# Optimization experiments

Measured on AMD Instinct MI355X. Metric: run time of the kernel, lower is better.

Reference implementation:

```python
import jax, jax.numpy as jnp
import numpy as np

# Config (decoder-only Transformer)
NL, H, D, DK, V, B, S = 6, 16, 1024, 64, 32000, 2, 1024  # DK = d_v = D // H
DFF = 4 * D


def _layer_norm(x, g, b, eps=1e-5):
    mu = jnp.mean(x, axis=-1, keepdims=True)
    var = jnp.mean(jnp.square(x - mu), axis=-1, keepdims=True)
    return (x - mu) * jax.lax.rsqrt(var + eps) * g + b


def _pos_encoding(seq_len, d_embed):
    # Matches PositionalEncoding: base 1000 (as in source), sin at even i, cos at odd i
    pos = jnp.arange(seq_len, dtype=jnp.float32)[:, None]
    i = jnp.arange(d_embed, dtype=jnp.float32)[None, :]
    angle = pos / jnp.power(1000.0, i / d_embed)
    return jnp.where((jnp.arange(d_embed)[None, :] % 2) == 0, jnp.sin(angle), jnp.cos(angle))


def setup_inputs() -> dict:
    key = jax.random.key(0)
    ks = jax.random.split(key, 8)
    n = lambda k, shp, sc: jax.random.normal(k, shp, dtype=jnp.float32) * sc
    return {
        "outputs": jax.random.randint(ks[0], (B, S), 0, V),
        "embed": n(ks[1], (V, D), 0.02),
        # per-head Q/K/V projections stacked over layers and heads: [NL, H, D, DK]
        "Wq": n(ks[2], (NL, H, D, DK), D ** -0.5),
        "Wk": n(ks[3], (NL, H, D, DK), D ** -0.5),
        "Wv": n(ks[4], (NL, H, D, DK), D ** -0.5),
        "W1": n(ks[5], (NL, D, DFF), D ** -0.5),
        "W2": n(ks[6], (NL, DFF, D), DFF ** -0.5),
        "ln1_g": jnp.ones((NL, D), jnp.float32),
        "ln1_b": jnp.zeros((NL, D), jnp.float32),
        "ln2_g": jnp.ones((NL, D), jnp.float32),
        "ln2_b": jnp.zeros((NL, D), jnp.float32),
        "Wout": n(ks[7], (D, V), D ** -0.5),
        "bout": jnp.zeros((V,), jnp.float32),
    }


def reference(outputs, embed, Wq, Wk, Wv, W1, W2, ln1_g, ln1_b, ln2_g, ln2_b, Wout, bout):
    x = embed[outputs]                      # [B, S, D]
    x = x + _pos_encoding(S, D)
    scale = jnp.float32(DK ** 0.5)
    for l in range(NL):
        # Masked multi-head self-attention (per-head projections batched over H)
        q = jnp.einsum('bsd,hdk->bhsk', x, Wq[l])
        k = jnp.einsum('bsd,hdk->bhsk', x, Wk[l])
        v = jnp.einsum('bsd,hdk->bhsk', x, Wv[l])
        scores = jnp.einsum('bhqk,bhsk->bhqs', q, k) / scale   # [B,H,S,S]
        # Faithful to source: tril then masked_fill(score == 0, -inf)
        scores = jnp.tril(scores)
        scores = jnp.where(scores == 0, -jnp.inf, scores)
        w = jax.nn.softmax(scores, axis=-1)
        attn = jnp.einsum('bhqs,bhsv->bqhv', w, v).reshape(B, S, H * DK)
        x = _layer_norm(x + attn, ln1_g[l], ln1_b[l])
        # Position-wise FFN (dropout is identity at inference)
        h = jax.nn.relu(x @ W1[l]) @ W2[l]
        x = _layer_norm(x + h, ln2_g[l], ln2_b[l])
    return x @ Wout + bout                  # logits [B, S, V]
```

## Files before the change

### kernel.cpp

```cpp
#include <hip/hip_runtime.h>

typedef unsigned short u16;
typedef __attribute__((ext_vector_type(8))) short short8;
typedef __attribute__((ext_vector_type(4))) float f32x4;

#define NLAYER 6
#define NH 16
#define DMODEL 1024
#define DHEAD 64
#define NVOCAB 32000
#define NB 2
#define NS 1024
#define NDFF 4096
#define MTOK (NB*NS)

__device__ __forceinline__ u16 f2b(float f) {
    union { float f; unsigned u; } x; x.f = f;
    unsigned r = x.u + 0x7fffu + ((x.u >> 16) & 1u);
    return (u16)(r >> 16);
}

#define GLL16(gp, lp) __builtin_amdgcn_global_load_lds( \
    (const __attribute__((address_space(1))) void*)(gp), \
    (__attribute__((address_space(3))) void*)(lp), 16, 0, 0)

__global__ void transpose_cvt(const float* __restrict__ src, u16* __restrict__ dst,
                              int R, int C, long srcStride, long dstStride)
{
    __shared__ float t[32][33];
    const int c0 = blockIdx.x * 32, r0 = blockIdx.y * 32;
    const float* s = src + (long)blockIdx.z * srcStride;
    u16* d = dst + (long)blockIdx.z * dstStride;
    const int tx = threadIdx.x, ty = threadIdx.y;
    #pragma unroll
    for (int j = 0; j < 32; j += 8)
        t[ty + j][tx] = s[(long)(r0 + ty + j) * C + c0 + tx];
    __syncthreads();
    #pragma unroll
    for (int j = 0; j < 32; j += 8)
        d[(long)(c0 + ty + j) * R + r0 + tx] = f2b(t[tx][ty + j]);
}

__global__ void transpose_qkv(const float* __restrict__ src, u16* __restrict__ dst, int sel)
{
    __shared__ float t[32][33];
    const int bi = blockIdx.z, l = bi >> 4, h = bi & 15;
    const float* s = src + (long)bi * (DMODEL * DHEAD);
    u16* d = dst + (long)l * 3072 * DMODEL + (long)(sel * 1024 + h * 64) * DMODEL;
    const int c0 = blockIdx.x * 32, r0 = blockIdx.y * 32;
    const int tx = threadIdx.x, ty = threadIdx.y;
    #pragma unroll
    for (int j = 0; j < 32; j += 8)
        t[ty + j][tx] = s[(long)(r0 + ty + j) * DHEAD + c0 + tx];
    __syncthreads();
    #pragma unroll
    for (int j = 0; j < 32; j += 8)
        d[(long)(c0 + ty + j) * DMODEL + r0 + tx] = f2b(t[tx][ty + j]);
}

__global__ void embed_pe(const int* __restrict__ toks, const float* __restrict__ emb,
                         float* __restrict__ x, u16* __restrict__ xb)
{
    const int row = blockIdx.x;
    const int s = row & (NS - 1);
    const long erow = (long)toks[row] * DMODEL;
    const long base = (long)row * DMODEL;
    #pragma unroll
    for (int j = 0; j < 4; ++j) {
        int d = threadIdx.x + j * 256;
        float ang = (float)s * exp2f(-(float)d * (9.965784284662087f / 1024.f));
        float pe = (d & 1) ? cosf(ang) : sinf(ang);
        float v = emb[erow + d] + pe;
        x[base + d] = v;
        xb[base + d] = f2b(v);
    }
}

template<int ND>
__global__ __launch_bounds__(256) void ln_residual(
    const float* __restrict__ xin, const float* __restrict__ delta,
    const float* __restrict__ delta2,
    const float* __restrict__ g, const float* __restrict__ bb,
    float* __restrict__ xout, u16* __restrict__ xbout)
{
    __shared__ float red[8];
    const long base = (long)blockIdx.x * DMODEL;
    float v[4]; float sum = 0.f, sq = 0.f;
    #pragma unroll
    for (int j = 0; j < 4; ++j) {
        int d = threadIdx.x + j * 256;
        float t = xin[base + d] + delta[base + d];
        if (ND == 2) t += delta2[base + d];
        v[j] = t; sum += t; sq += t * t;
    }
    #pragma unroll
    for (int off = 1; off < 64; off <<= 1) {
        sum += __shfl_xor(sum, off, 64);
        sq  += __shfl_xor(sq,  off, 64);
    }
    const int wv = threadIdx.x >> 6, lane = threadIdx.x & 63;
    if (lane == 0) { red[wv] = sum; red[4 + wv] = sq; }
    __syncthreads();
    float ts = red[0] + red[1] + red[2] + red[3];
    float tq = red[4] + red[5] + red[6] + red[7];
    float mu = ts * (1.f / DMODEL);
    float var = tq * (1.f / DMODEL) - mu * mu;
    float rstd = rsqrtf(var + 1e-5f);
    #pragma unroll
    for (int j = 0; j < 4; ++j) {
        int d = threadIdx.x + j * 256;
        float y = (v[j] - mu) * rstd * g[d] + bb[d];
        xout[base + d] = y;
        xbout[base + d] = f2b(y);
    }
}

template<int BM, int EPI>
__global__ __launch_bounds__(BM*2, 2) void gemm_pipe(
    const u16* __restrict__ A, const u16* __restrict__ Bt,
    void* __restrict__ Cout, const float* __restrict__ bias,
    int M, int N, int K, int lda, int ldb, size_t zstride)
{
    constexpr int WAVES = BM / 32;
    constexpr int WC = WAVES / 2;
    constexpr int MR = BM / 32;
    constexpr int TILE = BM * 32;

    __shared__ __align__(16) u16 As[4][TILE];
    __shared__ __align__(16) u16 Bs[4][TILE];

    const int nmb = M / BM;
    {
    }
    const int id = blockIdx.x, nwg = gridDim.x;
    const int q = nwg >> 3, r = nwg & 7, xcd = id & 7, loc = id >> 3;
    const int swz = (xcd < r ? xcd * (q + 1) : r * (q + 1) + (xcd - r) * q) + loc;
    const int m0 = (swz % nmb) * BM, n0 = (swz / nmb) * BM;
    const int koff = blockIdx.y * K;

    const int tid = threadIdx.x, wv = tid >> 6, lane = tid & 63;
    const int wr = wv / WC, wc = wv % WC;
    const int lrow = lane & 15, ks = lane >> 4;

    const u16* gsrc[4];
    int ldso[2];
    {
        const int l4 = lane >> 2, s = lane & 3;
        #pragma unroll
        for (int j = 0; j < 2; ++j) {
            const int row = j * (WAVES * 16) + wv * 16 + l4;
            const int x = (row >> 1) & 3;
            gsrc[j]     = A  + (size_t)(m0 + row) * lda + koff + (size_t)((s ^ x) * 8);
            gsrc[2 + j] = Bt + (size_t)(n0 + row) * ldb + koff + (size_t)((s ^ x) * 8);
            ldso[j] = (j * (WAVES * 16) + wv * 16) * 32;
        }
    }
    int aoff[MR], boff[4];
    #pragma unroll
    for (int m = 0; m < MR; ++m) {
        const int row = wr * (BM / 2) + m * 16 + lrow;
        aoff[m] = row * 32 + ((ks ^ ((row >> 1) & 3)) * 8);
    }
    #pragma unroll
    for (int n = 0; n < 4; ++n) {
        const int row = wc * 64 + n * 16 + lrow;
        boff[n] = row * 32 + ((ks ^ ((row >> 1) & 3)) * 8);
    }

    const int NT = K / 32;
    auto ISSUE = [&](int t) {
        const int b = t & 3;
        const size_t ko = (size_t)t * 32;
        #pragma unroll
        for (int j = 0; j < 2; ++j) {
            GLL16(gsrc[j] + ko,     &As[b][ldso[j]]);
            GLL16(gsrc[2 + j] + ko, &Bs[b][ldso[j]]);
        }
    };

    f32x4 acc[MR][4] = {};
    ISSUE(0); ISSUE(1); ISSUE(2);

    for (int t = 0; t < NT; ++t) {
        if (t < NT - 2)       { asm volatile("s_waitcnt vmcnt(8)" ::: "memory"); }
        else if (t == NT - 2) { asm volatile("s_waitcnt vmcnt(4)" ::: "memory"); }
        else                  { asm volatile("s_waitcnt vmcnt(0)" ::: "memory"); }
        __builtin_amdgcn_sched_barrier(0);
        __builtin_amdgcn_s_barrier();
        __builtin_amdgcn_sched_barrier(0);

        const int b = t & 3;
        short8 af[MR], bf[4];
        #pragma unroll
        for (int m = 0; m < MR; ++m) af[m] = *(const short8*)(&As[b][aoff[m]]);
        #pragma unroll
        for (int n = 0; n < 4; ++n)  bf[n] = *(const short8*)(&Bs[b][boff[n]]);
        if (t + 3 < NT) ISSUE(t + 3);
        __builtin_amdgcn_s_setprio(1);
        #pragma unroll
        for (int m = 0; m < MR; ++m)
            #pragma unroll
            for (int n = 0; n < 4; ++n)
                acc[m][n] = __builtin_amdgcn_mfma_f32_16x16x32_bf16(af[m], bf[n], acc[m][n], 0, 0, 0);
        __builtin_amdgcn_s_setprio(0);
    }

    #pragma unroll
    for (int m = 0; m < MR; ++m) {
        const int rr = m0 + wr * (BM / 2) + m * 16 + ks * 4;
        #pragma unroll
        for (int n = 0; n < 4; ++n) {
            const int cc = n0 + wc * 64 + n * 16 + lrow;
            if (EPI == 0) {
                float* C = (float*)Cout + (size_t)blockIdx.y * zstride;
                #pragma unroll
                for (int i = 0; i < 4; ++i) C[(size_t)(rr + i) * N + cc] = acc[m][n][i];
            } else if (EPI == 3) {
                float* C = (float*)Cout;
                const float bv = bias[cc];
                #pragma unroll
                for (int i = 0; i < 4; ++i) C[(size_t)(rr + i) * N + cc] = acc[m][n][i] + bv;
            } else {
                u16* C = (u16*)Cout;
                #pragma unroll
                for (int i = 0; i < 4; ++i) {
                    float vv = acc[m][n][i];
                    if (EPI == 2) vv = fmaxf(vv, 0.f);
                    C[(size_t)(rr + i) * N + cc] = f2b(vv);
                }
            }
        }
    }
}

__global__ __launch_bounds__(256, 2) void attn_flash(
    const u16* __restrict__ qkv, float* __restrict__ delta)
{
    __shared__ __align__(16) u16 Qs[64 * 64];
    __shared__ __align__(16) u16 Ks[64 * 64];
    __shared__ __align__(16) u16 Vts[64 * 64];
    __shared__ __align__(16) u16 Ps[4][16 * 64];

    const int pair = blockIdx.x, h = blockIdx.y, b = blockIdx.z;
    const int tid = threadIdx.x, wv = tid >> 6, lane = tid & 63;
    const int lrow = lane & 15, lk8 = (lane >> 4) * 8, li4 = (lane >> 4) * 4;
    const long base = (long)b * NS * 3072;

    for (int rep = 0; rep < 2; ++rep) {
        const int qt = rep == 0 ? pair : 15 - pair;
        __syncthreads();

        #pragma unroll
        for (int i = 0; i < 2; ++i) {
            int c0 = (wv * 2 + i) * 64;
            int c = c0 + lane;
            int row = c >> 3, col = (c & 7) * 8;
            GLL16(qkv + base + (long)(qt * 64 + row) * 3072 + h * 64 + col, Qs + c0 * 8);
        }

        f32x4 o[4] = {};
        float m_[4], l_[4];
        #pragma unroll
        for (int i = 0; i < 4; ++i) { m_[i] = -__builtin_inff(); l_[i] = 0.f; }

        for (int t = 0; t <= qt; ++t) {
            __syncthreads();
            #pragma unroll
            for (int i = 0; i < 2; ++i) {
                int c0 = (wv * 2 + i) * 64;
                int c = c0 + lane;
                int row = c >> 3, col = (c & 7) * 8;
                GLL16(qkv + base + (long)(t * 64 + row) * 3072 + 1024 + h * 64 + col, Ks + c0 * 8);
            }
            #pragma unroll
            for (int i = 0; i < 2; ++i) {
                int c = tid + i * 256;
                int kv = c >> 3, d0 = (c & 7) * 8;
                short8 vv = *(const short8*)(qkv + base + (long)(t * 64 + kv) * 3072 + 2048 + h * 64 + d0);
                #pragma unroll
                for (int j = 0; j < 8; ++j) Vts[(d0 + j) * 64 + kv] = ((u16*)&vv)[j];
            }
            __syncthreads();

            short8 aq[2];
            aq[0] = *(const short8*)(Qs + (wv * 16 + lrow) * 64 + lk8);
            aq[1] = *(const short8*)(Qs + (wv * 16 + lrow) * 64 + 32 + lk8);
            f32x4 sa[4];
            #pragma unroll
            for (int nb = 0; nb < 4; ++nb) {
                f32x4 z = {};
                #pragma unroll
                for (int kd = 0; kd < 2; ++kd) {
                    short8 bk = *(const short8*)(Ks + (nb * 16 + lrow) * 64 + kd * 32 + lk8);
                    z = __builtin_amdgcn_mfma_f32_16x16x32_bf16(aq[kd], bk, z, 0, 0, 0);
                }
                sa[nb] = z;
            }
            const int qrow0 = qt * 64 + wv * 16 + li4;
            #pragma unroll
            for (int nb = 0; nb < 4; ++nb)
                #pragma unroll
                for (int i = 0; i < 4; ++i) {
                    float sc = sa[nb][i] * 0.125f;
                    if (t == qt) {
                        int kvc = t * 64 + nb * 16 + lrow;
                        if (kvc > qrow0 + i) sc = -__builtin_inff();
                    }
                    sa[nb][i] = sc;
                }
            float mt[4];
            #pragma unroll
            for (int i = 0; i < 4; ++i)
                mt[i] = fmaxf(fmaxf(sa[0][i], sa[1][i]), fmaxf(sa[2][i], sa[3][i]));
            #pragma unroll
            for (int off = 1; off < 16; off <<= 1)
                #pragma unroll
                for (int i = 0; i < 4; ++i) mt[i] = fmaxf(mt[i], __shfl_xor(mt[i], off, 64));
            float fac[4], rs[4];
            #pragma unroll
            for (int i = 0; i < 4; ++i) {
                float mn = fmaxf(m_[i], mt[i]);
                fac[i] = expf(m_[i] - mn);
                m_[i] = mn;
                rs[i] = 0.f;
            }
            #pragma unroll
            for (int nb = 0; nb < 4; ++nb)
                #pragma unroll
                for (int i = 0; i < 4; ++i) {
                    float p = expf(sa[nb][i] - m_[i]);
                    sa[nb][i] = p; rs[i] += p;
                }
            #pragma unroll
            for (int off = 1; off < 16; off <<= 1)
                #pragma unroll
                for (int i = 0; i < 4; ++i) rs[i] += __shfl_xor(rs[i], off, 64);
            #pragma unroll
            for (int i = 0; i < 4; ++i) l_[i] = l_[i] * fac[i] + rs[i];
            #pragma unroll
            for (int nd = 0; nd < 4; ++nd)
                #pragma unroll
                for (int i = 0; i < 4; ++i) o[nd][i] *= fac[i];

            u16* ps = &Ps[wv][0];
            #pragma unroll
            for (int nb = 0; nb < 4; ++nb)
                #pragma unroll
                for (int i = 0; i < 4; ++i)
                    ps[(li4 + i) * 64 + nb * 16 + lrow] = f2b(sa[nb][i]);
            short8 pa[2];
            pa[0] = *(const short8*)(ps + lrow * 64 + lk8);
            pa[1] = *(const short8*)(ps + lrow * 64 + 32 + lk8);
            #pragma unroll
            for (int nd = 0; nd < 4; ++nd)
                #pragma unroll
                for (int kd = 0; kd < 2; ++kd) {
                    short8 vb = *(const short8*)(Vts + (nd * 16 + lrow) * 64 + kd * 32 + lk8);
                    o[nd] = __builtin_amdgcn_mfma_f32_16x16x32_bf16(pa[kd], vb, o[nd], 0, 0, 0);
                }
        }

        #pragma unroll
        for (int i = 0; i < 4; ++i) {
            const long row = (long)b * NS + qt * 64 + wv * 16 + li4 + i;
            const float inv = 1.f / l_[i];
            #pragma unroll
            for (int nd = 0; nd < 4; ++nd)
                delta[row * DMODEL + h * 64 + nd * 16 + lrow] = o[nd][i] * inv;
        }
    }
}

extern "C" void kernel_launch(void* const* d_in, const int* in_sizes, int n_in,
                              void* d_out, int out_size, void* d_ws, size_t ws_size,
                              hipStream_t stream) {
    const int*   toks  = (const int*)d_in[0];
    const float* emb   = (const float*)d_in[1];
    const float* Wq    = (const float*)d_in[2];
    const float* Wk    = (const float*)d_in[3];
    const float* Wv    = (const float*)d_in[4];
    const float* W1    = (const float*)d_in[5];
    const float* W2    = (const float*)d_in[6];
    const float* ln1g  = (const float*)d_in[7];
    const float* ln1b  = (const float*)d_in[8];
    const float* ln2g  = (const float*)d_in[9];
    const float* ln2b  = (const float*)d_in[10];
    const float* Wout  = (const float*)d_in[11];
    const float* bout  = (const float*)d_in[12];

    char* p = (char*)d_ws;
    auto alloc = [&](size_t bytes) { void* r = (void*)p; p += (bytes + 255) & ~(size_t)255; return r; };
    u16*   Wqkv_t = (u16*)alloc((size_t)NLAYER * 3072 * 1024 * 2);
    u16*   W1t    = (u16*)alloc((size_t)NLAYER * 4096 * 1024 * 2);
    u16*   W2t    = (u16*)alloc((size_t)NLAYER * 1024 * 4096 * 2);
    u16*   Woutt  = (u16*)alloc((size_t)NVOCAB * 1024 * 2);
    float* x      = (float*)alloc((size_t)MTOK * 1024 * 4);
    u16*   xb     = (u16*)alloc((size_t)MTOK * 1024 * 2);
    u16*   qkv    = (u16*)alloc((size_t)MTOK * 3072 * 2);
    u16*   hbuf   = (u16*)alloc((size_t)MTOK * 4096 * 2);
    float* dbuf   = (float*)alloc((size_t)MTOK * 1024 * 4);

    float* hbufF = (float*)hbuf;
    float* part2 = (float*)qkv;
    const size_t zstride = (size_t)(part2 - dbuf);

    dim3 tb(32, 8);
    transpose_qkv<<<dim3(2, 32, 96), tb, 0, stream>>>(Wq, Wqkv_t, 0);
    transpose_qkv<<<dim3(2, 32, 96), tb, 0, stream>>>(Wk, Wqkv_t, 1);
    transpose_qkv<<<dim3(2, 32, 96), tb, 0, stream>>>(Wv, Wqkv_t, 2);
    transpose_cvt<<<dim3(128, 32, 6), tb, 0, stream>>>(W1, W1t, 1024, 4096, 1024l * 4096, 4096l * 1024);
    transpose_cvt<<<dim3(32, 128, 6), tb, 0, stream>>>(W2, W2t, 4096, 1024, 4096l * 1024, 1024l * 4096);
    transpose_cvt<<<dim3(1000, 32, 1), tb, 0, stream>>>(Wout, Woutt, 1024, NVOCAB, 0, 0);

    embed_pe<<<MTOK, 256, 0, stream>>>(toks, emb, x, xb);

    for (int l = 0; l < NLAYER; ++l) {
        gemm_pipe<128, 1><<<dim3(16 * 24), 256, 0, stream>>>(
            xb, Wqkv_t + (size_t)l * 3072 * 1024, qkv, nullptr, MTOK, 3072, 1024, 1024, 1024, 0);
        attn_flash<<<dim3(8, NH, NB), 256, 0, stream>>>(qkv, hbufF);
        ln_residual<1><<<MTOK, 256, 0, stream>>>(x, hbufF, nullptr,
            ln1g + l * 1024, ln1b + l * 1024, x, xb);
        gemm_pipe<128, 2><<<dim3(16 * 32), 256, 0, stream>>>(
            xb, W1t + (size_t)l * 4096 * 1024, hbuf, nullptr, MTOK, 4096, 1024, 1024, 1024, 0);
        gemm_pipe<128, 0><<<dim3(16 * 8, 2), 256, 0, stream>>>(
            hbuf, W2t + (size_t)l * 1024 * 4096, dbuf, nullptr, MTOK, 1024, 2048, 4096, 4096, zstride);
        ln_residual<2><<<MTOK, 256, 0, stream>>>(x, dbuf, part2,
            ln2g + l * 1024, ln2b + l * 1024, x, xb);
    }

    gemm_pipe<256, 3><<<dim3(8 * 125), 512, 0, stream>>>(
        xb, Woutt, (float*)d_out, bout, MTOK, NVOCAB, 1024, 1024, 1024, 0);
}
```

Measured before the change: 1.305 ms.

## Double-buffer attention K/V with swizzled LDS, add dedicated vocab GEMM, vectorize transposes

Attention now double-buffers K and V tiles in LDS. The next tile's loads are prefetched into registers and the global-to-LDS path while the current tile computes, and XOR swizzling is applied to Q/K/V/P to avoid bank conflicts. A new 256x256 GEMM kernel for the output projection splits each k-step into two half-phases, interleaving B-tile prefetch with MFMAs and raising wave priority around the MFMA blocks. Weight transposes use 64x64 tiles with float4 loads and 16-byte stores. The added waitcnt and barrier choreography is intricate and could hide ordering bugs or raise register pressure.

New measurement: 1.451 ms. +11.1%, slower.

```diff
diff --git a/kernel.cpp b/kernel.cpp
--- a/kernel.cpp
+++ b/kernel.cpp
@@ -24,21 +24,34 @@
     (const __attribute__((address_space(1))) void*)(gp), \
     (__attribute__((address_space(3))) void*)(lp), 16, 0, 0)
 
-__global__ void transpose_cvt(const float* __restrict__ src, u16* __restrict__ dst,
-                              int R, int C, long srcStride, long dstStride)
+__global__ __launch_bounds__(256) void trans64(
+    const float* __restrict__ src, u16* __restrict__ dst,
+    int R, int C, long sStride, long dStride)
 {
-    __shared__ float t[32][33];
-    const int c0 = blockIdx.x * 32, r0 = blockIdx.y * 32;
-    const float* s = src + (long)blockIdx.z * srcStride;
-    u16* d = dst + (long)blockIdx.z * dstStride;
-    const int tx = threadIdx.x, ty = threadIdx.y;
-    #pragma unroll
-    for (int j = 0; j < 32; j += 8)
-        t[ty + j][tx] = s[(long)(r0 + ty + j) * C + c0 + tx];
+    __shared__ float sh[64][65];
+    const int c0 = blockIdx.x * 64, r0 = blockIdx.y * 64;
+    const float* s = src + (long)blockIdx.z * sStride;
+    u16* d = dst + (long)blockIdx.z * dStride;
+    const int tid = threadIdx.x;
+    const int lr = tid >> 4, lc = (tid & 15) * 4;
+    #pragma unroll
+    for (int q = 0; q < 4; ++q) {
+        const float4 v = *(const float4*)(s + (long)(r0 + q * 16 + lr) * C + c0 + lc);
+        sh[q * 16 + lr][lc + 0] = v.x;
+        sh[q * 16 + lr][lc + 1] = v.y;
+        sh[q * 16 + lr][lc + 2] = v.z;
+        sh[q * 16 + lr][lc + 3] = v.w;
+    }
     __syncthreads();
     #pragma unroll
-    for (int j = 0; j < 32; j += 8)
-        d[(long)(c0 + ty + j) * R + r0 + tx] = f2b(t[tx][ty + j]);
+    for (int k = 0; k < 2; ++k) {
+        const int t = tid + 256 * k;
+        const int col = t >> 3, rch = (t & 7) * 8;
+        u16 tmp[8];
+        #pragma unroll
+        for (int j = 0; j < 8; ++j) tmp[j] = f2b(sh[rch + j][col]);
+        *(short8*)(d + (long)(c0 + col) * R + r0 + rch) = *(const short8*)tmp;
+    }
 }
 
 __global__ void transpose_qkv(const float* __restrict__ src, u16* __restrict__ dst, int sel)
@@ -130,8 +143,6 @@
     __shared__ __align__(16) u16 Bs[4][TILE];
 
     const int nmb = M / BM;
-    {
-    }
     const int id = blockIdx.x, nwg = gridDim.x;
     const int q = nwg >> 3, r = nwg & 7, xcd = id & 7, loc = id >> 3;
     const int swz = (xcd < r ? xcd * (q + 1) : r * (q + 1) + (xcd - r) * q) + loc;
@@ -233,17 +244,126 @@
     }
 }
 
-__global__ __launch_bounds__(256, 2) void attn_flash(
+__global__ __launch_bounds__(512, 2) void gemm256(
+    const u16* __restrict__ A, const u16* __restrict__ Bt,
+    float* __restrict__ C, const float* __restrict__ bias,
+    int M, int N, int K)
+{
+    __shared__ __align__(16) u16 As[4][256 * 32];
+    __shared__ __align__(16) u16 Bs[4][256 * 32];
+
+    const int nmb = M >> 8;
+    const int id = blockIdx.x, nwg = gridDim.x;
+    const int q = nwg >> 3, r = nwg & 7, xcd = id & 7, loc = id >> 3;
+    const int swz = (xcd < r ? xcd * (q + 1) : r * (q + 1) + (xcd - r) * q) + loc;
+    const int m0 = (swz % nmb) * 256, n0 = (swz / nmb) * 256;
+
+    const int tid = threadIdx.x, wv = tid >> 6, lane = tid & 63;
+    const int wr = wv >> 2, wc = wv & 3;
+    const int lrow = lane & 15, ks = lane >> 4;
+
+    const u16* srcA[2]; const u16* srcB[2]; int dsto[2];
+    #pragma unroll
+    for (int i = 0; i < 2; ++i) {
+        const int c = (wv * 2 + i) * 64 + lane;
+        const int row = c >> 2, up = c & 3;
+        const int u = up ^ ((row >> 1) & 3);
+        srcA[i] = A  + (size_t)(m0 + row) * K + u * 8;
+        srcB[i] = Bt + (size_t)(n0 + row) * K + u * 8;
+        dsto[i] = c * 8;
+    }
+    int aoff[8], boff[4];
+    #pragma unroll
+    for (int m = 0; m < 8; ++m) {
+        const int row = wr * 128 + m * 16 + lrow;
+        aoff[m] = row * 32 + ((ks ^ ((row >> 1) & 3)) * 8);
+    }
+    #pragma unroll
+    for (int n = 0; n < 4; ++n) {
+        const int row = wc * 64 + n * 16 + lrow;
+        boff[n] = row * 32 + ((ks ^ ((row >> 1) & 3)) * 8);
+    }
+
+    const int NT = K >> 5;
+    for (int t = 0; t < 3; ++t) {
+        const int b = t & 3;
+        #pragma unroll
+        for (int i = 0; i < 2; ++i) GLL16(srcA[i] + t * 32, &As[b][dsto[i]]);
+        #pragma unroll
+        for (int i = 0; i < 2; ++i) GLL16(srcB[i] + t * 32, &Bs[b][dsto[i]]);
+    }
+
+    f32x4 acc[8][4] = {};
+    for (int t = 0; t < NT; ++t) {
+        const int b = t & 3, bs = (t + 3) & 3;
+        if (t < NT - 2)       { asm volatile("s_waitcnt vmcnt(8)" ::: "memory"); }
+        else if (t == NT - 2) { asm volatile("s_waitcnt vmcnt(4)" ::: "memory"); }
+        else                  { asm volatile("s_waitcnt vmcnt(0)" ::: "memory"); }
+        __builtin_amdgcn_sched_barrier(0);
+        __builtin_amdgcn_s_barrier();
+        __builtin_amdgcn_sched_barrier(0);
+
+        short8 af[4], bf[4];
+        #pragma unroll
+        for (int m = 0; m < 4; ++m) af[m] = *(const short8*)(&As[b][aoff[m]]);
+        #pragma unroll
+        for (int n = 0; n < 4; ++n) bf[n] = *(const short8*)(&Bs[b][boff[n]]);
+        if (t + 3 < NT) {
+            #pragma unroll
+            for (int i = 0; i < 2; ++i) GLL16(srcA[i] + (t + 3) * 32, &As[bs][dsto[i]]);
+        }
+        __builtin_amdgcn_s_setprio(1);
+        #pragma unroll
+        for (int m = 0; m < 4; ++m)
+            #pragma unroll
+            for (int n = 0; n < 4; ++n)
+                acc[m][n] = __builtin_amdgcn_mfma_f32_16x16x32_bf16(af[m], bf[n], acc[m][n], 0, 0, 0);
+        __builtin_amdgcn_s_setprio(0);
+
+        __builtin_amdgcn_sched_barrier(0);
+        __builtin_amdgcn_s_barrier();
+        __builtin_amdgcn_sched_barrier(0);
+
+        short8 af2[4];
+        #pragma unroll
+        for (int m = 0; m < 4; ++m) af2[m] = *(const short8*)(&As[b][aoff[4 + m]]);
+        if (t + 3 < NT) {
+            #pragma unroll
+            for (int i = 0; i < 2; ++i) GLL16(srcB[i] + (t + 3) * 32, &Bs[bs][dsto[i]]);
+        }
+        __builtin_amdgcn_s_setprio(1);
+        #pragma unroll
+        for (int m = 0; m < 4; ++m)
+            #pragma unroll
+            for (int n = 0; n < 4; ++n)
+                acc[4 + m][n] = __builtin_amdgcn_mfma_f32_16x16x32_bf16(af2[m], bf[n], acc[4 + m][n], 0, 0, 0);
+        __builtin_amdgcn_s_setprio(0);
+    }
+
+    #pragma unroll
+    for (int m = 0; m < 8; ++m) {
+        const int rr = m0 + wr * 128 + m * 16 + ks * 4;
+        #pragma unroll
+        for (int n = 0; n < 4; ++n) {
+            const int cc = n0 + wc * 64 + n * 16 + lrow;
+            const float bv = bias[cc];
+            #pragma unroll
+            for (int i = 0; i < 4; ++i) C[(size_t)(rr + i) * N + cc] = acc[m][n][i] + bv;
+        }
+    }
+}
+
+__global__ __launch_bounds__(256, 3) void attn_flash2(
     const u16* __restrict__ qkv, float* __restrict__ delta)
 {
     __shared__ __align__(16) u16 Qs[64 * 64];
-    __shared__ __align__(16) u16 Ks[64 * 64];
-    __shared__ __align__(16) u16 Vts[64 * 64];
+    __shared__ __align__(16) u16 Kd[2][64 * 64];
+    __shared__ __align__(16) u16 Vd[2][64 * 64];
     __shared__ __align__(16) u16 Ps[4][16 * 64];
 
     const int pair = blockIdx.x, h = blockIdx.y, b = blockIdx.z;
     const int tid = threadIdx.x, wv = tid >> 6, lane = tid & 63;
-    const int lrow = lane & 15, lk8 = (lane >> 4) * 8, li4 = (lane >> 4) * 4;
+    const int lrow = lane & 15, ks4 = lane >> 4, li4 = ks4 * 4;
     const long base = (long)b * NS * 3072;
 
     for (int rep = 0; rep < 2; ++rep) {
@@ -252,10 +372,44 @@
 
         #pragma unroll
         for (int i = 0; i < 2; ++i) {
-            int c0 = (wv * 2 + i) * 64;
-            int c = c0 + lane;
-            int row = c >> 3, col = (c & 7) * 8;
-            GLL16(qkv + base + (long)(qt * 64 + row) * 3072 + h * 64 + col, Qs + c0 * 8);
+            const int c = (wv * 2 + i) * 64 + lane;
+            const int row = c >> 3, u = (c & 7) ^ (row & 7);
+            GLL16(qkv + base + (long)(qt * 64 + row) * 3072 + h * 64 + u * 8, Qs + c * 8);
+        }
+        short8 vreg[2];
+        #pragma unroll
+        for (int i = 0; i < 2; ++i) {
+            const int c = tid + 256 * i;
+            vreg[i] = *(const short8*)(qkv + base + (long)(c >> 3) * 3072 + 2048 + h * 64 + (c & 7) * 8);
+        }
+        #pragma unroll
+        for (int i = 0; i < 2; ++i) {
+            const int c = (wv * 2 + i) * 64 + lane;
+            const int row = c >> 3, u = (c & 7) ^ (row & 7);
+            GLL16(qkv + base + (long)(row) * 3072 + 1024 + h * 64 + u * 8, Kd[0] + c * 8);
+        }
+        asm volatile("s_waitcnt vmcnt(4)" ::: "memory");
+        __builtin_amdgcn_sched_barrier(0);
+        __builtin_amdgcn_s_barrier();
+        __builtin_amdgcn_sched_barrier(0);
+        short8 aq[2];
+        {
+            const int row = wv * 16 + lrow;
+            aq[0] = *(const short8*)(Qs + row * 64 + ((ks4 ^ (row & 7)) * 8));
+            aq[1] = *(const short8*)(Qs + row * 64 + (((4 + ks4) ^ (row & 7)) * 8));
+        }
+        asm volatile("s_waitcnt vmcnt(2)" ::: "memory");
+        __builtin_amdgcn_sched_barrier(0);
+        #pragma unroll
+        for (int i = 0; i < 2; ++i) {
+            const int c = tid + 256 * i;
+            const int kv = c >> 3, d0 = (c & 7) * 8;
+            #pragma unroll
+            for (int jj = 0; jj < 8; ++jj) {
+                const int j = jj ^ (lane & 7);
+                const int row = d0 + j;
+                Vd[0][row * 64 + (((kv >> 3) ^ (row & 7)) * 8) + (kv & 7)] = ((const u16*)&vreg[i])[j];
+            }
         }
 
         f32x4 o[4] = {};
@@ -264,34 +418,39 @@
         for (int i = 0; i < 4; ++i) { m_[i] = -__builtin_inff(); l_[i] = 0.f; }
 
         for (int t = 0; t <= qt; ++t) {
-            __syncthreads();
-            #pragma unroll
-            for (int i = 0; i < 2; ++i) {
-                int c0 = (wv * 2 + i) * 64;
-                int c = c0 + lane;
-                int row = c >> 3, col = (c & 7) * 8;
-                GLL16(qkv + base + (long)(t * 64 + row) * 3072 + 1024 + h * 64 + col, Ks + c0 * 8);
+            const int p = t & 1;
+            asm volatile("s_waitcnt lgkmcnt(0)" ::: "memory");
+            __builtin_amdgcn_sched_barrier(0);
+            __builtin_amdgcn_s_barrier();
+            __builtin_amdgcn_sched_barrier(0);
+
+            short8 vnext[2];
+            if (t < qt) {
+                #pragma unroll
+                for (int i = 0; i < 2; ++i) {
+                    const int c = tid + 256 * i;
+                    vnext[i] = *(const short8*)(qkv + base + (long)((t + 1) * 64 + (c >> 3)) * 3072 + 2048 + h * 64 + (c & 7) * 8);
+                }
+                #pragma unroll
+                for (int i = 0; i < 2; ++i) {
+                    const int c = (wv * 2 + i) * 64 + lane;
+                    const int row = c >> 3, u = (c & 7) ^ (row & 7);
+                    GLL16(qkv + base + (long)((t + 1) * 64 + row) * 3072 + 1024 + h * 64 + u * 8, Kd[p ^ 1] + c * 8);
+                }
+                asm volatile("s_waitcnt vmcnt(4)" ::: "memory");
+            } else {
+                asm volatile("s_waitcnt vmcnt(0)" ::: "memory");
             }
-            #pragma unroll
-            for (int i = 0; i < 2; ++i) {
-                int c = tid + i * 256;
-                int kv = c >> 3, d0 = (c & 7) * 8;
-                short8 vv = *(const short8*)(qkv + base + (long)(t * 64 + kv) * 3072 + 2048 + h * 64 + d0);
-                #pragma unroll
-                for (int j = 0; j < 8; ++j) Vts[(d0 + j) * 64 + kv] = ((u16*)&vv)[j];
-            }
-            __syncthreads();
-
-            short8 aq[2];
-            aq[0] = *(const short8*)(Qs + (wv * 16 + lrow) * 64 + lk8);
-            aq[1] = *(const short8*)(Qs + (wv * 16 + lrow) * 64 + 32 + lk8);
+            __builtin_amdgcn_sched_barrier(0);
+
             f32x4 sa[4];
             #pragma unroll
             for (int nb = 0; nb < 4; ++nb) {
                 f32x4 z = {};
                 #pragma unroll
                 for (int kd = 0; kd < 2; ++kd) {
-                    short8 bk = *(const short8*)(Ks + (nb * 16 + lrow) * 64 + kd * 32 + lk8);
+                    const int row = nb * 16 + lrow;
+                    short8 bk = *(const short8*)(Kd[p] + row * 64 + (((kd * 4 + ks4) ^ (row & 7)) * 8));
                     z = __builtin_amdgcn_mfma_f32_16x16x32_bf16(aq[kd], bk, z, 0, 0, 0);
                 }
                 sa[nb] = z;
@@ -328,8 +487,8 @@
             for (int nb = 0; nb < 4; ++nb)
                 #pragma unroll
                 for (int i = 0; i < 4; ++i) {
-                    float p = expf(sa[nb][i] - m_[i]);
-                    sa[nb][i] = p; rs[i] += p;
+                    float pp = expf(sa[nb][i] - m_[i]);
+                    sa[nb][i] = pp; rs[i] += pp;
                 }
             #pragma unroll
             for (int off = 1; off < 16; off <<= 1)
@@ -346,16 +505,34 @@
             #pragma unroll
             for (int nb = 0; nb < 4; ++nb)
                 #pragma unroll
-                for (int i = 0; i < 4; ++i)
-                    ps[(li4 + i) * 64 + nb * 16 + lrow] = f2b(sa[nb][i]);
+                for (int i = 0; i < 4; ++i) {
+                    const int row = li4 + i, col = nb * 16 + lrow;
+                    ps[row * 64 + (((col >> 3) ^ (row & 7)) * 8) + (col & 7)] = f2b(sa[nb][i]);
+                }
+            if (t < qt) {
+                asm volatile("s_waitcnt vmcnt(2)" ::: "memory");
+                __builtin_amdgcn_sched_barrier(0);
+                #pragma unroll
+                for (int i = 0; i < 2; ++i) {
+                    const int c = tid + 256 * i;
+                    const int kv = c >> 3, d0 = (c & 7) * 8;
+                    #pragma unroll
+                    for (int jj = 0; jj < 8; ++jj) {
+                        const int j = jj ^ (lane & 7);
+                        const int row = d0 + j;
+                        Vd[p ^ 1][row * 64 + (((kv >> 3) ^ (row & 7)) * 8) + (kv & 7)] = ((const u16*)&vnext[i])[j];
+                    }
+                }
+            }
             short8 pa[2];
-            pa[0] = *(const short8*)(ps + lrow * 64 + lk8);
-            pa[1] = *(const short8*)(ps + lrow * 64 + 32 + lk8);
+            pa[0] = *(const short8*)(ps + lrow * 64 + ((ks4 ^ (lrow & 7)) * 8));
+            pa[1] = *(const short8*)(ps + lrow * 64 + (((4 + ks4) ^ (lrow & 7)) * 8));
             #pragma unroll
             for (int nd = 0; nd < 4; ++nd)
                 #pragma unroll
                 for (int kd = 0; kd < 2; ++kd) {
-                    short8 vb = *(const short8*)(Vts + (nd * 16 + lrow) * 64 + kd * 32 + lk8);
+                    const int row = nd * 16 + lrow;
+                    short8 vb = *(const short8*)(Vd[p] + row * 64 + (((kd * 4 + ks4) ^ (row & 7)) * 8));
                     o[nd] = __builtin_amdgcn_mfma_f32_16x16x32_bf16(pa[kd], vb, o[nd], 0, 0, 0);
                 }
         }
@@ -404,20 +581,19 @@
     float* part2 = (float*)qkv;
     const size_t zstride = (size_t)(part2 - dbuf);
 
-    dim3 tb(32, 8);
-    transpose_qkv<<<dim3(2, 32, 96), tb, 0, stream>>>(Wq, Wqkv_t, 0);
-    transpose_qkv<<<dim3(2, 32, 96), tb, 0, stream>>>(Wk, Wqkv_t, 1);
-    transpose_qkv<<<dim3(2, 32, 96), tb, 0, stream>>>(Wv, Wqkv_t, 2);
-    transpose_cvt<<<dim3(128, 32, 6), tb, 0, stream>>>(W1, W1t, 1024, 4096, 1024l * 4096, 4096l * 1024);
-    transpose_cvt<<<dim3(32, 128, 6), tb, 0, stream>>>(W2, W2t, 4096, 1024, 4096l * 1024, 1024l * 4096);
-    transpose_cvt<<<dim3(1000, 32, 1), tb, 0, stream>>>(Wout, Woutt, 1024, NVOCAB, 0, 0);
+    transpose_qkv<<<dim3(2, 32, 96), dim3(32, 8), 0, stream>>>(Wq, Wqkv_t, 0);
+    transpose_qkv<<<dim3(2, 32, 96), dim3(32, 8), 0, stream>>>(Wk, Wqkv_t, 1);
+    transpose_qkv<<<dim3(2, 32, 96), dim3(32, 8), 0, stream>>>(Wv, Wqkv_t, 2);
+    trans64<<<dim3(64, 16, 6), 256, 0, stream>>>(W1, W1t, 1024, 4096, 1024l * 4096, 4096l * 1024);
+    trans64<<<dim3(16, 64, 6), 256, 0, stream>>>(W2, W2t, 4096, 1024, 4096l * 1024, 1024l * 4096);
+    trans64<<<dim3(500, 16, 1), 256, 0, stream>>>(Wout, Woutt, 1024, NVOCAB, 0, 0);
 
     embed_pe<<<MTOK, 256, 0, stream>>>(toks, emb, x, xb);
 
     for (int l = 0; l < NLAYER; ++l) {
         gemm_pipe<128, 1><<<dim3(16 * 24), 256, 0, stream>>>(
             xb, Wqkv_t + (size_t)l * 3072 * 1024, qkv, nullptr, MTOK, 3072, 1024, 1024, 1024, 0);
-        attn_flash<<<dim3(8, NH, NB), 256, 0, stream>>>(qkv, hbufF);
+        attn_flash2<<<dim3(8, NH, NB), 256, 0, stream>>>(qkv, hbufF);
         ln_residual<1><<<MTOK, 256, 0, stream>>>(x, hbufF, nullptr,
             ln1g + l * 1024, ln1b + l * 1024, x, xb);
         gemm_pipe<128, 2><<<dim3(16 * 32), 256, 0, stream>>>(
@@ -428,6 +604,6 @@
             ln2g + l * 1024, ln2b + l * 1024, x, xb);
     }
 
-    gemm_pipe<256, 3><<<dim3(8 * 125), 512, 0, stream>>>(
-        xb, Woutt, (float*)d_out, bout, MTOK, NVOCAB, 1024, 1024, 1024, 0);
-}
+    gemm256<<<dim3(8 * 125), 512, 0, stream>>>(
+        xb, Woutt, (float*)d_out, bout, MTOK, NVOCAB, 1024);
+}
```

## Swizzle attention LDS, vectorize transposes and fp32 GEMM epilogue, split-K 4

Applied to the files above, without the earlier changes.

The weight transpose kernels move to 64x64 tiles that read with float4 and write 16-byte bf16 vectors. The fp32 GEMM epilogues now stage each accumulator tile through LDS so rows go out as coalesced float4 stores. The attention kernel gets XOR-swizzled LDS layouts for Q, K, V^T and P to avoid bank conflicts, and loads Q fragments once per query tile. The W2 GEMM goes from 2-way to 4-way split-K, with the LayerNorm summing four partials, and the vocab projection switches from 256 to 128 tiles. These trade extra LDS traffic and more partial-buffer reads and writes for better memory coalescing and more parallelism.

Result: no change. 1.288 ms (-1.4%).

```diff
diff --git a/kernel.cpp b/kernel.cpp
--- a/kernel.cpp
+++ b/kernel.cpp
@@ -24,21 +24,34 @@
     (const __attribute__((address_space(1))) void*)(gp), \
     (__attribute__((address_space(3))) void*)(lp), 16, 0, 0)
 
-__global__ void transpose_cvt(const float* __restrict__ src, u16* __restrict__ dst,
-                              int R, int C, long srcStride, long dstStride)
-{
-    __shared__ float t[32][33];
-    const int c0 = blockIdx.x * 32, r0 = blockIdx.y * 32;
-    const float* s = src + (long)blockIdx.z * srcStride;
-    u16* d = dst + (long)blockIdx.z * dstStride;
-    const int tx = threadIdx.x, ty = threadIdx.y;
-    #pragma unroll
-    for (int j = 0; j < 32; j += 8)
-        t[ty + j][tx] = s[(long)(r0 + ty + j) * C + c0 + tx];
+__global__ __launch_bounds__(256) void trans64(
+    const float* __restrict__ src, u16* __restrict__ dst,
+    int R, int C, long sStride, long dStride)
+{
+    __shared__ float sh[64][65];
+    const int c0 = blockIdx.x * 64, r0 = blockIdx.y * 64;
+    const float* s = src + (long)blockIdx.z * sStride;
+    u16* d = dst + (long)blockIdx.z * dStride;
+    const int tid = threadIdx.x;
+    const int lr = tid >> 4, lc = (tid & 15) * 4;
+    #pragma unroll
+    for (int q = 0; q < 4; ++q) {
+        const float4 v = *(const float4*)(s + (long)(r0 + q * 16 + lr) * C + c0 + lc);
+        sh[q * 16 + lr][lc + 0] = v.x;
+        sh[q * 16 + lr][lc + 1] = v.y;
+        sh[q * 16 + lr][lc + 2] = v.z;
+        sh[q * 16 + lr][lc + 3] = v.w;
+    }
     __syncthreads();
     #pragma unroll
-    for (int j = 0; j < 32; j += 8)
-        d[(long)(c0 + ty + j) * R + r0 + tx] = f2b(t[tx][ty + j]);
+    for (int k = 0; k < 2; ++k) {
+        const int t = tid + 256 * k;
+        const int col = t >> 3, rch = (t & 7) * 8;
+        u16 tmp[8];
+        #pragma unroll
+        for (int j = 0; j < 8; ++j) tmp[j] = f2b(sh[rch + j][col]);
+        *(short8*)(d + (long)(c0 + col) * R + r0 + rch) = *(const short8*)tmp;
+    }
 }
 
 __global__ void transpose_qkv(const float* __restrict__ src, u16* __restrict__ dst, int sel)
@@ -78,8 +91,7 @@
 
 template<int ND>
 __global__ __launch_bounds__(256) void ln_residual(
-    const float* __restrict__ xin, const float* __restrict__ delta,
-    const float* __restrict__ delta2,
+    const float* __restrict__ xin, const float* __restrict__ delta, size_t pstride,
     const float* __restrict__ g, const float* __restrict__ bb,
     float* __restrict__ xout, u16* __restrict__ xbout)
 {
@@ -89,8 +101,9 @@
     #pragma unroll
     for (int j = 0; j < 4; ++j) {
         int d = threadIdx.x + j * 256;
-        float t = xin[base + d] + delta[base + d];
-        if (ND == 2) t += delta2[base + d];
+        float t = xin[base + d];
+        #pragma unroll
+        for (int y = 0; y < ND; ++y) t += delta[base + (size_t)y * pstride + d];
         v[j] = t; sum += t; sq += t * t;
     }
     #pragma unroll
@@ -130,8 +143,6 @@
     __shared__ __align__(16) u16 Bs[4][TILE];
 
     const int nmb = M / BM;
-    {
-    }
     const int id = blockIdx.x, nwg = gridDim.x;
     const int q = nwg >> 3, r = nwg & 7, xcd = id & 7, loc = id >> 3;
     const int swz = (xcd < r ? xcd * (q + 1) : r * (q + 1) + (xcd - r) * q) + loc;
@@ -205,23 +216,38 @@
         __builtin_amdgcn_s_setprio(0);
     }
 
-    #pragma unroll
-    for (int m = 0; m < MR; ++m) {
-        const int rr = m0 + wr * (BM / 2) + m * 16 + ks * 4;
-        #pragma unroll
-        for (int n = 0; n < 4; ++n) {
-            const int cc = n0 + wc * 64 + n * 16 + lrow;
-            if (EPI == 0) {
-                float* C = (float*)Cout + (size_t)blockIdx.y * zstride;
-                #pragma unroll
-                for (int i = 0; i < 4; ++i) C[(size_t)(rr + i) * N + cc] = acc[m][n][i];
-            } else if (EPI == 3) {
-                float* C = (float*)Cout;
-                const float bv = bias[cc];
-                #pragma unroll
-                for (int i = 0; i < 4; ++i) C[(size_t)(rr + i) * N + cc] = acc[m][n][i] + bv;
-            } else {
-                u16* C = (u16*)Cout;
+    if (EPI == 0 || EPI == 3) {
+        __syncthreads();
+        float* patch = (float*)((BM == 256 && (wv & 4)) ? (void*)&Bs[0][0] : (void*)&As[0][0])
+                       + (wv & 3) * (16 * 68);
+        const int cc0 = n0 + wc * 64;
+        f32x4 bvv = {};
+        if (EPI == 3) bvv = *(const f32x4*)(bias + cc0 + (lane & 15) * 4);
+        float* C = (float*)Cout + (EPI == 0 ? (size_t)blockIdx.y * zstride : (size_t)0);
+        #pragma unroll
+        for (int m = 0; m < MR; ++m) {
+            #pragma unroll
+            for (int n = 0; n < 4; ++n)
+                #pragma unroll
+                for (int i = 0; i < 4; ++i)
+                    patch[(ks * 4 + i) * 68 + n * 16 + lrow] = acc[m][n][i];
+            #pragma unroll
+            for (int i2 = 0; i2 < 4; ++i2) {
+                const int prow = i2 * 4 + ks;
+                f32x4 v = *(const f32x4*)(patch + prow * 68 + (lane & 15) * 4);
+                if (EPI == 3) v += bvv;
+                const int rr = m0 + wr * (BM / 2) + m * 16 + prow;
+                *(f32x4*)(C + (size_t)rr * N + cc0 + (lane & 15) * 4) = v;
+            }
+        }
+    } else {
+        u16* C = (u16*)Cout;
+        #pragma unroll
+        for (int m = 0; m < MR; ++m) {
+            const int rr = m0 + wr * (BM / 2) + m * 16 + ks * 4;
+            #pragma unroll
+            for (int n = 0; n < 4; ++n) {
+                const int cc = n0 + wc * 64 + n * 16 + lrow;
                 #pragma unroll
                 for (int i = 0; i < 4; ++i) {
                     float vv = acc[m][n][i];
@@ -233,7 +259,7 @@
     }
 }
 
-__global__ __launch_bounds__(256, 2) void attn_flash(
+__global__ __launch_bounds__(256, 2) void attn_flash3(
     const u16* __restrict__ qkv, float* __restrict__ delta)
 {
     __shared__ __align__(16) u16 Qs[64 * 64];
@@ -243,19 +269,25 @@
 
     const int pair = blockIdx.x, h = blockIdx.y, b = blockIdx.z;
     const int tid = threadIdx.x, wv = tid >> 6, lane = tid & 63;
-    const int lrow = lane & 15, lk8 = (lane >> 4) * 8, li4 = (lane >> 4) * 4;
+    const int lrow = lane & 15, ks4 = lane >> 4, li4 = ks4 * 4;
     const long base = (long)b * NS * 3072;
 
     for (int rep = 0; rep < 2; ++rep) {
-        const int qt = rep == 0 ? pair : 15 - pair;
+        const int qt = rep ? 15 - pair : pair;
         __syncthreads();
 
         #pragma unroll
         for (int i = 0; i < 2; ++i) {
-            int c0 = (wv * 2 + i) * 64;
-            int c = c0 + lane;
-            int row = c >> 3, col = (c & 7) * 8;
-            GLL16(qkv + base + (long)(qt * 64 + row) * 3072 + h * 64 + col, Qs + c0 * 8);
+            const int c = (wv * 2 + i) * 64 + lane;
+            const int row = c >> 3, u = (c & 7) ^ (row & 7);
+            GLL16(qkv + base + (long)(qt * 64 + row) * 3072 + h * 64 + u * 8, Qs + c * 8);
+        }
+        __syncthreads();
+        short8 aq[2];
+        {
+            const int row = wv * 16 + lrow;
+            aq[0] = *(const short8*)(Qs + row * 64 + ((ks4 ^ (row & 7)) * 8));
+            aq[1] = *(const short8*)(Qs + row * 64 + (((4 + ks4) ^ (row & 7)) * 8));
         }
 
         f32x4 o[4] = {};
@@ -267,31 +299,32 @@
             __syncthreads();
             #pragma unroll
             for (int i = 0; i < 2; ++i) {
-                int c0 = (wv * 2 + i) * 64;
-                int c = c0 + lane;
-                int row = c >> 3, col = (c & 7) * 8;
-                GLL16(qkv + base + (long)(t * 64 + row) * 3072 + 1024 + h * 64 + col, Ks + c0 * 8);
+                const int c = (wv * 2 + i) * 64 + lane;
+                const int row = c >> 3, u = (c & 7) ^ (row & 7);
+                GLL16(qkv + base + (long)(t * 64 + row) * 3072 + 1024 + h * 64 + u * 8, Ks + c * 8);
             }
             #pragma unroll
             for (int i = 0; i < 2; ++i) {
-                int c = tid + i * 256;
-                int kv = c >> 3, d0 = (c & 7) * 8;
+                const int c = tid + 256 * i;
+                const int kv = c >> 3, d0 = (c & 7) * 8;
                 short8 vv = *(const short8*)(qkv + base + (long)(t * 64 + kv) * 3072 + 2048 + h * 64 + d0);
                 #pragma unroll
-                for (int j = 0; j < 8; ++j) Vts[(d0 + j) * 64 + kv] = ((u16*)&vv)[j];
+                for (int jj = 0; jj < 8; ++jj) {
+                    const int j = jj ^ (lane & 7);
+                    const int row = d0 + j;
+                    Vts[row * 64 + (((kv >> 3) ^ (row & 7)) * 8) + (kv & 7)] = ((const u16*)&vv)[j];
+                }
             }
             __syncthreads();
 
-            short8 aq[2];
-            aq[0] = *(const short8*)(Qs + (wv * 16 + lrow) * 64 + lk8);
-            aq[1] = *(const short8*)(Qs + (wv * 16 + lrow) * 64 + 32 + lk8);
             f32x4 sa[4];
             #pragma unroll
             for (int nb = 0; nb < 4; ++nb) {
                 f32x4 z = {};
                 #pragma unroll
                 for (int kd = 0; kd < 2; ++kd) {
-                    short8 bk = *(const short8*)(Ks + (nb * 16 + lrow) * 64 + kd * 32 + lk8);
+                    const int row = nb * 16 + lrow;
+                    short8 bk = *(const short8*)(Ks + row * 64 + (((kd * 4 + ks4) ^ (row & 7)) * 8));
                     z = __builtin_amdgcn_mfma_f32_16x16x32_bf16(aq[kd], bk, z, 0, 0, 0);
                 }
                 sa[nb] = z;
@@ -328,8 +361,8 @@
             for (int nb = 0; nb < 4; ++nb)
                 #pragma unroll
                 for (int i = 0; i < 4; ++i) {
-                    float p = expf(sa[nb][i] - m_[i]);
-                    sa[nb][i] = p; rs[i] += p;
+                    float pp = expf(sa[nb][i] - m_[i]);
+                    sa[nb][i] = pp; rs[i] += pp;
                 }
             #pragma unroll
             for (int off = 1; off < 16; off <<= 1)
@@ -346,16 +379,19 @@
             #pragma unroll
             for (int nb = 0; nb < 4; ++nb)
                 #pragma unroll
-                for (int i = 0; i < 4; ++i)
-                    ps[(li4 + i) * 64 + nb * 16 + lrow] = f2b(sa[nb][i]);
+                for (int i = 0; i < 4; ++i) {
+                    const int row = li4 + i, col = nb * 16 + lrow;
+                    ps[row * 64 + (((col >> 3) ^ (row & 7)) * 8) + (col & 7)] = f2b(sa[nb][i]);
+                }
             short8 pa[2];
-            pa[0] = *(const short8*)(ps + lrow * 64 + lk8);
-            pa[1] = *(const short8*)(ps + lrow * 64 + 32 + lk8);
+            pa[0] = *(const short8*)(ps + lrow * 64 + ((ks4 ^ (lrow & 7)) * 8));
+            pa[1] = *(const short8*)(ps + lrow * 64 + (((4 + ks4) ^ (lrow & 7)) * 8));
             #pragma unroll
             for (int nd = 0; nd < 4; ++nd)
                 #pragma unroll
                 for (int kd = 0; kd < 2; ++kd) {
-                    short8 vb = *(const short8*)(Vts + (nd * 16 + lrow) * 64 + kd * 32 + lk8);
+                    const int row = nd * 16 + lrow;
+                    short8 vb = *(const short8*)(Vts + row * 64 + (((kd * 4 + ks4) ^ (row & 7)) * 8));
                     o[nd] = __builtin_amdgcn_mfma_f32_16x16x32_bf16(pa[kd], vb, o[nd], 0, 0, 0);
                 }
         }
@@ -390,6 +426,7 @@
 
     char* p = (char*)d_ws;
     auto alloc = [&](size_t bytes) { void* r = (void*)p; p += (bytes + 255) & ~(size_t)255; return r; };
+    const size_t PSZ = (size_t)MTOK * 1024;
     u16*   Wqkv_t = (u16*)alloc((size_t)NLAYER * 3072 * 1024 * 2);
     u16*   W1t    = (u16*)alloc((size_t)NLAYER * 4096 * 1024 * 2);
     u16*   W2t    = (u16*)alloc((size_t)NLAYER * 1024 * 4096 * 2);
@@ -398,36 +435,33 @@
     u16*   xb     = (u16*)alloc((size_t)MTOK * 1024 * 2);
     u16*   qkv    = (u16*)alloc((size_t)MTOK * 3072 * 2);
     u16*   hbuf   = (u16*)alloc((size_t)MTOK * 4096 * 2);
-    float* dbuf   = (float*)alloc((size_t)MTOK * 1024 * 4);
+    float* dbuf   = (float*)alloc(PSZ * 4 * 4);
 
     float* hbufF = (float*)hbuf;
-    float* part2 = (float*)qkv;
-    const size_t zstride = (size_t)(part2 - dbuf);
-
-    dim3 tb(32, 8);
-    transpose_qkv<<<dim3(2, 32, 96), tb, 0, stream>>>(Wq, Wqkv_t, 0);
-    transpose_qkv<<<dim3(2, 32, 96), tb, 0, stream>>>(Wk, Wqkv_t, 1);
-    transpose_qkv<<<dim3(2, 32, 96), tb, 0, stream>>>(Wv, Wqkv_t, 2);
-    transpose_cvt<<<dim3(128, 32, 6), tb, 0, stream>>>(W1, W1t, 1024, 4096, 1024l * 4096, 4096l * 1024);
-    transpose_cvt<<<dim3(32, 128, 6), tb, 0, stream>>>(W2, W2t, 4096, 1024, 4096l * 1024, 1024l * 4096);
-    transpose_cvt<<<dim3(1000, 32, 1), tb, 0, stream>>>(Wout, Woutt, 1024, NVOCAB, 0, 0);
+
+    transpose_qkv<<<dim3(2, 32, 96), dim3(32, 8), 0, stream>>>(Wq, Wqkv_t, 0);
+    transpose_qkv<<<dim3(2, 32, 96), dim3(32, 8), 0, stream>>>(Wk, Wqkv_t, 1);
+    transpose_qkv<<<dim3(2, 32, 96), dim3(32, 8), 0, stream>>>(Wv, Wqkv_t, 2);
+    trans64<<<dim3(64, 16, 6), 256, 0, stream>>>(W1, W1t, 1024, 4096, 1024l * 4096, 4096l * 1024);
+    trans64<<<dim3(16, 64, 6), 256, 0, stream>>>(W2, W2t, 4096, 1024, 4096l * 1024, 1024l * 4096);
+    trans64<<<dim3(500, 16, 1), 256, 0, stream>>>(Wout, Woutt, 1024, NVOCAB, 0, 0);
 
     embed_pe<<<MTOK, 256, 0, stream>>>(toks, emb, x, xb);
 
     for (int l = 0; l < NLAYER; ++l) {
         gemm_pipe<128, 1><<<dim3(16 * 24), 256, 0, stream>>>(
             xb, Wqkv_t + (size_t)l * 3072 * 1024, qkv, nullptr, MTOK, 3072, 1024, 1024, 1024, 0);
-        attn_flash<<<dim3(8, NH, NB), 256, 0, stream>>>(qkv, hbufF);
-        ln_residual<1><<<MTOK, 256, 0, stream>>>(x, hbufF, nullptr,
+        attn_flash3<<<dim3(8, NH, NB), 256, 0, stream>>>(qkv, hbufF);
+        ln_residual<1><<<MTOK, 256, 0, stream>>>(x, hbufF, 0,
             ln1g + l * 1024, ln1b + l * 1024, x, xb);
         gemm_pipe<128, 2><<<dim3(16 * 32), 256, 0, stream>>>(
             xb, W1t + (size_t)l * 4096 * 1024, hbuf, nullptr, MTOK, 4096, 1024, 1024, 1024, 0);
-        gemm_pipe<128, 0><<<dim3(16 * 8, 2), 256, 0, stream>>>(
-            hbuf, W2t + (size_t)l * 1024 * 4096, dbuf, nullptr, MTOK, 1024, 2048, 4096, 4096, zstride);
-        ln_residual<2><<<MTOK, 256, 0, stream>>>(x, dbuf, part2,
+        gemm_pipe<128, 0><<<dim3(16 * 8, 4), 256, 0, stream>>>(
+            hbuf, W2t + (size_t)l * 1024 * 4096, dbuf, nullptr, MTOK, 1024, 1024, 4096, 4096, PSZ);
+        ln_residual<4><<<MTOK, 256, 0, stream>>>(x, dbuf, PSZ,
             ln2g + l * 1024, ln2b + l * 1024, x, xb);
     }
 
-    gemm_pipe<256, 3><<<dim3(8 * 125), 512, 0, stream>>>(
+    gemm_pipe<128, 3><<<dim3(16 * 250), 256, 0, stream>>>(
         xb, Woutt, (float*)d_out, bout, MTOK, NVOCAB, 1024, 1024, 1024, 0);
 }
```
